# Kernel optimization log

Measured on AMD Instinct MI355X. Metric: run time of the kernel, lower is better.

## Reference

```python
import math
import jax, jax.numpy as jnp
import numpy as np

EMBED_DIM = 2048
NUM_HEADS = 16
DEPTH = 12
LAMBDA_INIT = 0.8 - 0.6 * math.exp(-0.3 * DEPTH)
LN_EPS = 1e-5


def setup_inputs() -> dict:
    key = jax.random.key(0)
    ks = jax.random.split(key, 9)
    D = EMBED_DIM
    hd = D // NUM_HEADS // 2  # 64
    B, T = 1, 2048
    w_std = D ** -0.5
    return {
        "x": jax.random.normal(ks[0], (B, T, D), jnp.float32),
        "Wq": jax.random.normal(ks[1], (D, D), jnp.float32) * w_std,
        "Wk": jax.random.normal(ks[2], (D, D), jnp.float32) * w_std,
        "Wv": jax.random.normal(ks[3], (D, D), jnp.float32) * w_std,
        "Wo": jax.random.normal(ks[4], (D, D), jnp.float32) * w_std,
        "lambda_q1": jax.random.normal(ks[5], (hd,), jnp.float32) * 0.1,
        "lambda_k1": jax.random.normal(ks[6], (hd,), jnp.float32) * 0.1,
        "lambda_q2": jax.random.normal(ks[7], (hd,), jnp.float32) * 0.1,
        "lambda_k2": jax.random.normal(ks[8], (hd,), jnp.float32) * 0.1,
    }


def reference(x, Wq, Wk, Wv, Wo, lambda_q1, lambda_k1, lambda_q2, lambda_k2):
    B, T, D = x.shape
    hd = lambda_q1.shape[0]
    H = D // (2 * hd)  # num_heads
    scale = hd ** -0.5

    # projections (torch Linear, no bias); n_rep == 1 so k/v are full width
    q = (x @ Wq).reshape(B, T, 2 * H, hd).transpose(0, 2, 1, 3) * scale  # (B,2H,T,hd)
    k = (x @ Wk).reshape(B, T, 2 * H, hd).transpose(0, 2, 1, 3)          # (B,2H,T,hd)
    v = (x @ Wv).reshape(B, T, H, 2 * hd).transpose(0, 2, 1, 3)          # (B,H,T,2hd)

    # dual-stream attention logits with causal mask (offset = 0)
    attn = jnp.einsum("bhqd,bhkd->bhqk", q, k)  # (B,2H,T,T)
    mask = jnp.triu(jnp.full((T, T), -jnp.inf, dtype=attn.dtype), 1)
    attn = jax.nn.softmax((attn + mask).astype(jnp.float32), axis=-1).astype(x.dtype)

    # lambda reparameterization
    lam1 = jnp.exp(jnp.sum(lambda_q1 * lambda_k1))
    lam2 = jnp.exp(jnp.sum(lambda_q2 * lambda_k2))
    lam = lam1 - lam2 + LAMBDA_INIT

    attn = attn.reshape(B, H, 2, T, T)
    diff = attn[:, :, 0] - lam * attn[:, :, 1]  # (B,H,T,T)
    out = jnp.einsum("bhqk,bhkd->bhqd", diff, v)  # (B,H,T,2hd)

    # subln: LayerNorm over last dim (2hd), no affine, biased variance
    mu = jnp.mean(out, axis=-1, keepdims=True)
    var = jnp.mean(jnp.square(out - mu), axis=-1, keepdims=True)
    out = (out - mu) / jnp.sqrt(var + LN_EPS)
    out = out * (1.0 - LAMBDA_INIT)

    # NOTE: faithful to original -- reshape WITHOUT transposing heads back
    out = out.reshape(B, T, H * 2 * hd)
    return out @ Wo
```

## Files before the change

kernel.cpp:

```cpp
#include <hip/hip_runtime.h>
#include <hip/hip_bf16.h>


typedef unsigned short u16;
typedef __attribute__((ext_vector_type(4))) float f32x4;
typedef __attribute__((ext_vector_type(8))) short bf16x8;

#define LAMBDA_INIT  0.7836057665317954f
#define ONE_MINUS_LI 0.2163942334682046f
#define QSCALE 0.18033688011112042f

#define EXP2F(x) __builtin_amdgcn_exp2f(x)

__device__ __forceinline__ u16 f2bf(float f) {
    union { float f; unsigned u; } v; v.f = f;
    unsigned r = v.u + 0x7FFFu + ((v.u >> 16) & 1u);
    return (u16)(r >> 16);
}

__device__ __forceinline__ unsigned pkbf(float a, float b) {
    union { __hip_bfloat162 h; unsigned u; } c;
    c.h = __float22bfloat162_rn(make_float2(a, b));
    return c.u;
}

__device__ __forceinline__ void gld_lds16(const u16* g, u16* l) {
    __builtin_amdgcn_global_load_lds((const __attribute__((address_space(1))) void*)g,
                                     (__attribute__((address_space(3))) void*)l, 16, 0, 0);
}

__global__ void cast_f32_bf16(const float* __restrict__ in, u16* __restrict__ out) {
    int i = (blockIdx.x * 256 + threadIdx.x) * 4;
    float4 v = *(const float4*)(in + i);
    uint2 o;
    o.x = pkbf(v.x, v.y);
    o.y = pkbf(v.z, v.w);
    *(uint2*)(out + i) = o;
}

__global__ void transpose_cast4(const float* __restrict__ W0, const float* __restrict__ W1,
                                const float* __restrict__ W2, const float* __restrict__ W3,
                                u16* __restrict__ O0, u16* __restrict__ O1,
                                u16* __restrict__ O2, u16* __restrict__ O3) {
    __shared__ float tile[64][65];
    const int z = blockIdx.z;
    const float* W = z == 0 ? W0 : z == 1 ? W1 : z == 2 ? W2 : W3;
    u16* Wt = z == 0 ? O0 : z == 1 ? O1 : z == 2 ? O2 : O3;
    const int c0 = blockIdx.x * 64, r0 = blockIdx.y * 64;
    const int t = threadIdx.x;
    const int lr = t >> 2, lc = (t & 3) << 4;
#pragma unroll
    for (int jj = 0; jj < 4; jj++) {
        float4 v = *(const float4*)(W + (size_t)(r0 + lr) * 2048 + c0 + lc + 4 * jj);
        tile[lr][lc + 4 * jj + 0] = v.x;
        tile[lr][lc + 4 * jj + 1] = v.y;
        tile[lr][lc + 4 * jj + 2] = v.z;
        tile[lr][lc + 4 * jj + 3] = v.w;
    }
    __syncthreads();
    const int oc = t >> 2, op = (t & 3) << 4;
    uint ou[8];
#pragma unroll
    for (int k = 0; k < 8; k++)
        ou[k] = pkbf(tile[op + 2 * k][oc], tile[op + 2 * k + 1][oc]);
    u16* dst = Wt + (size_t)(c0 + oc) * 2048 + r0 + op;
    *(uint4*)(dst) = *(uint4*)&ou[0];
    *(uint4*)(dst + 8) = *(uint4*)&ou[4];
}

__device__ __forceinline__ void gemm_core32(const u16* __restrict__ A, const u16* __restrict__ B,
                                            u16* __restrict__ Cout, float scale, int m0, int n0) {
    __shared__ __align__(16) u16 As[2][128 * 32];
    __shared__ __align__(16) u16 Bs[2][64 * 32];
    const int tid = threadIdx.x;
    const int lane = tid & 63, w = tid >> 6;
    const int q16 = lane & 15, g = lane >> 4;
    const int sl = (g ^ q16) & 3;
    const f32x4 fzero = {0.f, 0.f, 0.f, 0.f};
    f32x4 acc[2][4];
#pragma unroll
    for (int m = 0; m < 2; m++)
#pragma unroll
        for (int n = 0; n < 4; n++) acc[m][n] = fzero;

#define STG32(buf, kb)                                                               \
    {                                                                                \
        _Pragma("unroll") for (int p = 0; p < 2; p++) {                              \
            int s = p * 256 + tid;                              \
            int row = s >> 2, sg = (s ^ row) & 3;                                    \
            gld_lds16(A + (size_t)(m0 + row) * 2048 + (kb) + sg * 8, As[buf] + s * 8); \
        }                                                                            \
        {                                                                            \
            int s = tid;                                        \
            int row = s >> 2, sg = (s ^ row) & 3;                                    \
            gld_lds16(B + (size_t)(n0 + row) * 2048 + (kb) + sg * 8, Bs[buf] + s * 8); \
        }                                                                            \
    }

    STG32(0, 0);
    int cur = 0;
    for (int kb = 0; kb < 2048; kb += 32) {
        if (kb + 32 < 2048) {
            STG32(cur ^ 1, kb + 32);
            asm volatile("s_waitcnt vmcnt(3)" ::: "memory");
        } else {
            asm volatile("s_waitcnt vmcnt(0)" ::: "memory");
        }
        __builtin_amdgcn_s_barrier();
        bf16x8 af[2], bfr[4];
#pragma unroll
        for (int m = 0; m < 2; m++)
            af[m] = *(const bf16x8*)(As[cur] + (w * 32 + m * 16 + q16) * 32 + 8 * sl);
#pragma unroll
        for (int n = 0; n < 4; n++)
            bfr[n] = *(const bf16x8*)(Bs[cur] + (n * 16 + q16) * 32 + 8 * sl);
        __builtin_amdgcn_s_setprio(1);
#pragma unroll
        for (int m = 0; m < 2; m++)
#pragma unroll
            for (int n = 0; n < 4; n++)
                acc[m][n] = __builtin_amdgcn_mfma_f32_16x16x32_bf16(af[m], bfr[n], acc[m][n], 0, 0, 0);
        __builtin_amdgcn_s_setprio(0);
        asm volatile("s_waitcnt lgkmcnt(0)" ::: "memory");
        __builtin_amdgcn_s_barrier();
        cur ^= 1;
    }
#pragma unroll
    for (int m = 0; m < 2; m++)
#pragma unroll
        for (int n = 0; n < 4; n++) {
            int row = m0 + w * 32 + m * 16 + 4 * g;
            int col = n0 + n * 16 + q16;
#pragma unroll
            for (int r = 0; r < 4; r++)
                Cout[(size_t)(row + r) * 2048 + col] = f2bf(acc[m][n][r] * scale);
        }
#undef STG32
}

__device__ __forceinline__ void gemm_core64(const u16* __restrict__ A, const u16* __restrict__ B,
                                            float* __restrict__ Cout, float scale, int m0, int n0) {
    __shared__ __align__(16) u16 As[2][128 * 64];
    __shared__ __align__(16) u16 Bs[2][64 * 64];
    const int tid = threadIdx.x;
    const int lane = tid & 63, w = tid >> 6;
    const int q16 = lane & 15, g = lane >> 4;
    const int sw = q16 & 7;
    const f32x4 fzero = {0.f, 0.f, 0.f, 0.f};
    f32x4 acc[2][4];
#pragma unroll
    for (int m = 0; m < 2; m++)
#pragma unroll
        for (int n = 0; n < 4; n++) acc[m][n] = fzero;

#define STG64(buf, kb)                                                               \
    {                                                                                \
        _Pragma("unroll") for (int p = 0; p < 4; p++) {                              \
            int s = p * 256 + tid;                             \
            int row = s >> 3, sg = (s ^ row) & 7;                                    \
            gld_lds16(A + (size_t)(m0 + row) * 2048 + (kb) + sg * 8, As[buf] + s * 8); \
        }                                                                            \
        _Pragma("unroll") for (int p = 0; p < 2; p++) {                              \
            int s = p * 256 + tid;                              \
            int row = s >> 3, sg = (s ^ row) & 7;                                    \
            gld_lds16(B + (size_t)(n0 + row) * 2048 + (kb) + sg * 8, Bs[buf] + s * 8); \
        }                                                                            \
    }

    STG64(0, 0);
    int cur = 0;
    for (int kb = 0; kb < 2048; kb += 64) {
        if (kb + 64 < 2048) {
            STG64(cur ^ 1, kb + 64);
            asm volatile("s_waitcnt vmcnt(6)" ::: "memory");
        } else {
            asm volatile("s_waitcnt vmcnt(0)" ::: "memory");
        }
        __builtin_amdgcn_s_barrier();
        bf16x8 af[2][2], bfr[4][2];
#pragma unroll
        for (int m = 0; m < 2; m++) {
            const u16* ar = As[cur] + (w * 32 + m * 16 + q16) * 64;
            af[m][0] = *(const bf16x8*)(ar + 8 * (g ^ sw));
            af[m][1] = *(const bf16x8*)(ar + 8 * ((4 + g) ^ sw));
        }
#pragma unroll
        for (int n = 0; n < 4; n++) {
            const u16* br = Bs[cur] + (n * 16 + q16) * 64;
            bfr[n][0] = *(const bf16x8*)(br + 8 * (g ^ sw));
            bfr[n][1] = *(const bf16x8*)(br + 8 * ((4 + g) ^ sw));
        }
        __builtin_amdgcn_s_setprio(1);
#pragma unroll
        for (int m = 0; m < 2; m++)
#pragma unroll
            for (int n = 0; n < 4; n++) {
                acc[m][n] = __builtin_amdgcn_mfma_f32_16x16x32_bf16(af[m][0], bfr[n][0], acc[m][n], 0, 0, 0);
                acc[m][n] = __builtin_amdgcn_mfma_f32_16x16x32_bf16(af[m][1], bfr[n][1], acc[m][n], 0, 0, 0);
            }
        __builtin_amdgcn_s_setprio(0);
        asm volatile("s_waitcnt lgkmcnt(0)" ::: "memory");
        __builtin_amdgcn_s_barrier();
        cur ^= 1;
    }
#pragma unroll
    for (int m = 0; m < 2; m++)
#pragma unroll
        for (int n = 0; n < 4; n++) {
            int row = m0 + w * 32 + m * 16 + 4 * g;
            int col = n0 + n * 16 + q16;
#pragma unroll
            for (int r = 0; r < 4; r++)
                Cout[(size_t)(row + r) * 2048 + col] = acc[m][n][r] * scale;
        }
#undef STG64
}

__global__ __launch_bounds__(256, 6) void gemm_qkv(const u16* __restrict__ xb,
                                                   const u16* __restrict__ Wqt, const u16* __restrict__ Wkt,
                                                   const u16* __restrict__ Wvt,
                                                   u16* __restrict__ Qb, u16* __restrict__ Kb,
                                                   u16* __restrict__ Vtb) {
    const int id = blockIdx.x;
    const int ord = (id & 7) * 192 + (id >> 3);
    const int which = ord / 512, r = ord & 511;
    const int m0 = (r & 15) * 128, n0 = (r >> 4) * 64;
    const u16 *A, *B; u16* C; float sc;
    if (which == 0)      { A = xb;  B = Wqt; C = Qb;  sc = QSCALE; }
    else if (which == 1) { A = xb;  B = Wkt; C = Kb;  sc = 1.f; }
    else                 { A = Wvt; B = xb;  C = Vtb; sc = 1.f; }
    gemm_core32(A, B, C, sc, m0, n0);
}

__global__ __launch_bounds__(256, 3) void gemm_out(const u16* __restrict__ Mb, const u16* __restrict__ Wot,
                                                   float* __restrict__ out) {
    const int id = blockIdx.x;
    const int ord = (id & 7) * 64 + (id >> 3);
    const int m0 = (ord & 15) * 128, n0 = (ord >> 4) * 64;
    gemm_core64(Mb, Wot, out, 1.f, m0, n0);
}

__global__ __launch_bounds__(256, 2) void diff_attn(const u16* __restrict__ Qg, const u16* __restrict__ Kg,
                                                    const u16* __restrict__ Vg, u16* __restrict__ Mg,
                                                    const float* __restrict__ lq1, const float* __restrict__ lk1,
                                                    const float* __restrict__ lq2, const float* __restrict__ lk2) {
    __shared__ __align__(16) u16 smem[40960];
    const int tid = threadIdx.x;
    const int lane = tid & 63, w = tid >> 6;
    const int q16 = lane & 15, g = lane >> 4;
    const int sw = q16 & 7;
    const int id = blockIdx.x;
    const int xcd = id & 7, jj = id >> 3;
    const int p = jj >> 1, o = jj & 1;
    const int A = (p < 16) ? (32 - p) : (p - 15);
    const int s = o ? (33 - A) : A;
    const int qi = s - 1;
    const int h = (xcd << 1) | o;
    const int q0 = qi * 64;
    const int qg = q0 + 16 * w + q16;

    u16* Kb0 = smem;
    u16* Vb0 = smem + 8192;
    u16* Kb1 = smem + 16384;
    u16* Vb1 = smem + 24576;
    u16* Pw = smem + 32768 + w * 2048;

    bf16x8 qf[2][2];
#pragma unroll
    for (int st = 0; st < 2; st++)
#pragma unroll
        for (int db = 0; db < 2; db++)
            qf[st][db] = *(const bf16x8*)(Qg + (size_t)qg * 2048 + 128 * h + 64 * st + 32 * db + 8 * g);

#define STAGE_K(dst, kb)                                                         \
    {                                                                            \
        _Pragma("unroll") for (int p2 = 0; p2 < 4; p2++) {                       \
            int s2 = p2 * 256 + tid;                                             \
            int row = s2 >> 4, gc = s2 & 15;                                     \
            int sg = (gc ^ row) & 15;                                            \
            gld_lds16(Kg + (size_t)((kb) + row) * 2048 + 128 * h + sg * 8, (dst) + s2 * 8); \
        }                                                                        \
    }
#define STAGE_V(dst, kb)                                                         \
    {                                                                            \
        _Pragma("unroll") for (int p2 = 0; p2 < 4; p2++) {                       \
            int s2 = p2 * 256 + tid;                                             \
            int row = s2 >> 3, sg = (s2 ^ row) & 7;                              \
            gld_lds16(Vg + (size_t)(128 * h + row) * 2048 + (kb) + sg * 8, (dst) + s2 * 8); \
        }                                                                        \
    }

    const f32x4 fzero = {0.f, 0.f, 0.f, 0.f};
    f32x4 Oacc[2][8];
#pragma unroll
    for (int st = 0; st < 2; st++)
#pragma unroll
        for (int dt = 0; dt < 8; dt++) Oacc[st][dt] = fzero;
    float den[2] = {0.f, 0.f};

    const int nt = qi + 1;
    STAGE_K(Kb0, 0);
    STAGE_V(Vb0, 0);
    int cur = 0;
    for (int t = 0; t < nt; t++) {
        const int kb = t * 64;
        const u16* Ks = cur ? Kb1 : Kb0;
        const u16* Vs = cur ? Vb1 : Vb0;
        if (t + 1 < nt) {
            STAGE_K(cur ? Kb0 : Kb1, kb + 64);
            STAGE_V(cur ? Vb0 : Vb1, kb + 64);
            asm volatile("s_waitcnt vmcnt(8)" ::: "memory");
        } else {
            asm volatile("s_waitcnt vmcnt(0)" ::: "memory");
        }
        __builtin_amdgcn_s_barrier();

        f32x4 sc[2][4];
        __builtin_amdgcn_s_setprio(1);
#pragma unroll
        for (int st = 0; st < 2; st++)
#pragma unroll
            for (int kt = 0; kt < 4; kt++) {
                const u16* kr = Ks + (kt * 16 + q16) * 128;
                bf16x8 kf0 = *(const bf16x8*)(kr + 8 * ((st * 8 + g) ^ q16));
                bf16x8 kf1 = *(const bf16x8*)(kr + 8 * ((st * 8 + 4 + g) ^ q16));
                f32x4 a = __builtin_amdgcn_mfma_f32_16x16x32_bf16(kf0, qf[st][0], fzero, 0, 0, 0);
                a = __builtin_amdgcn_mfma_f32_16x16x32_bf16(kf1, qf[st][1], a, 0, 0, 0);
                sc[st][kt] = a;
            }
        __builtin_amdgcn_s_setprio(0);

        const bool last = (t == nt - 1);
#pragma unroll
        for (int st = 0; st < 2; st++) {
            u16* Pst = Pw + st * 1024;
            float dl = 0.f;
#pragma unroll
            for (int kt = 0; kt < 4; kt++) {
                float p0 = EXP2F(sc[st][kt][0]);
                float p1 = EXP2F(sc[st][kt][1]);
                float p2 = EXP2F(sc[st][kt][2]);
                float p3 = EXP2F(sc[st][kt][3]);
                if (last) {
                    const int kgi = kb + kt * 16 + 4 * g;
                    p0 = (kgi + 0 <= qg) ? p0 : 0.f;
                    p1 = (kgi + 1 <= qg) ? p1 : 0.f;
                    p2 = (kgi + 2 <= qg) ? p2 : 0.f;
                    p3 = (kgi + 3 <= qg) ? p3 : 0.f;
                }
                dl += (p0 + p1) + (p2 + p3);
                uint2 pr;
                pr.x = pkbf(p0, p1);
                pr.y = pkbf(p2, p3);
                *(uint2*)(Pst + q16 * 64 + ((kt * 16 + 4 * g) ^ (8 * sw))) = pr;
            }
            den[st] += dl;
        }

        bf16x8 pf[2][2];
#pragma unroll
        for (int st = 0; st < 2; st++)
#pragma unroll
            for (int kh = 0; kh < 2; kh++)
                pf[st][kh] = *(const bf16x8*)(Pw + st * 1024 + q16 * 64 + ((kh * 32 + 8 * g) ^ (8 * sw)));
        __builtin_amdgcn_s_setprio(1);
#pragma unroll
        for (int kh = 0; kh < 2; kh++)
#pragma unroll
            for (int dt = 0; dt < 8; dt++) {
                bf16x8 vf = *(const bf16x8*)(Vs + (dt * 16 + q16) * 64 + 8 * ((kh * 4 + g) ^ sw));
                Oacc[0][dt] = __builtin_amdgcn_mfma_f32_16x16x32_bf16(vf, pf[0][kh], Oacc[0][dt], 0, 0, 0);
                Oacc[1][dt] = __builtin_amdgcn_mfma_f32_16x16x32_bf16(vf, pf[1][kh], Oacc[1][dt], 0, 0, 0);
            }
        __builtin_amdgcn_s_setprio(0);
        asm volatile("s_waitcnt lgkmcnt(0)" ::: "memory");
        __builtin_amdgcn_s_barrier();
        cur ^= 1;
    }
#undef STAGE_K
#undef STAGE_V

    float sl1 = 0.f, sl2 = 0.f;
    for (int i = 0; i < 64; i++) { sl1 += lq1[i] * lk1[i]; sl2 += lq2[i] * lk2[i]; }
    const float lam = expf(sl1) - expf(sl2) + LAMBDA_INIT;

    float d0 = den[0], d1 = den[1];
    d0 += __shfl_xor(d0, 16); d0 += __shfl_xor(d0, 32);
    d1 += __shfl_xor(d1, 16); d1 += __shfl_xor(d1, 32);
    const float i1 = 1.f / d0;
    const float i2 = lam / d1;
    float S1 = 0.f, S2 = 0.f;
#pragma unroll
    for (int dt = 0; dt < 8; dt++)
#pragma unroll
        for (int r = 0; r < 4; r++) {
            float v = Oacc[0][dt][r] * i1 - Oacc[1][dt][r] * i2;
            S1 += v; S2 += v * v;
        }
    S1 += __shfl_xor(S1, 16); S1 += __shfl_xor(S1, 32);
    S2 += __shfl_xor(S2, 16); S2 += __shfl_xor(S2, 32);
    const float mu = S1 * (1.f / 128.f);
    const float var = S2 * (1.f / 128.f) - mu * mu;
    const float rs = rsqrtf(var + 1e-5f) * ONE_MINUS_LI;

    const int R = h * 128 + (q0 >> 4) + w;
    u16* drow = Mg + (size_t)R * 2048 + q16 * 128;
#pragma unroll
    for (int dt = 0; dt < 8; dt++) {
        float v0 = (Oacc[0][dt][0] * i1 - Oacc[1][dt][0] * i2 - mu) * rs;
        float v1 = (Oacc[0][dt][1] * i1 - Oacc[1][dt][1] * i2 - mu) * rs;
        float v2 = (Oacc[0][dt][2] * i1 - Oacc[1][dt][2] * i2 - mu) * rs;
        float v3 = (Oacc[0][dt][3] * i1 - Oacc[1][dt][3] * i2 - mu) * rs;
        uint2 oo;
        oo.x = pkbf(v0, v1);
        oo.y = pkbf(v2, v3);
        *(uint2*)(drow + dt * 16 + 4 * g) = oo;
    }
}

extern "C" void kernel_launch(void* const* d_in, const int* in_sizes, int n_in,
                              void* d_out, int out_size, void* d_ws, size_t ws_size,
                              hipStream_t stream) {
    (void)in_sizes; (void)n_in; (void)out_size; (void)ws_size;
    const float* x = (const float*)d_in[0];
    const float* Wq = (const float*)d_in[1];
    const float* Wk = (const float*)d_in[2];
    const float* Wv = (const float*)d_in[3];
    const float* Wo = (const float*)d_in[4];
    const float* lq1 = (const float*)d_in[5];
    const float* lk1 = (const float*)d_in[6];
    const float* lq2 = (const float*)d_in[7];
    const float* lk2 = (const float*)d_in[8];

    u16* ws = (u16*)d_ws;
    const size_t SZ = 2048u * 2048u;
    u16* xb = ws;
    u16* Wqt = ws + SZ;
    u16* Wkt = ws + 2 * SZ;
    u16* Wvt = ws + 3 * SZ;
    u16* Wot = ws + 4 * SZ;
    u16* Qb = ws + 5 * SZ;
    u16* Kb = ws + 6 * SZ;
    u16* Vtb = ws + 7 * SZ;
    u16* Mb = ws + 8 * SZ;

    cast_f32_bf16<<<4096, 256, 0, stream>>>(x, xb);
    transpose_cast4<<<dim3(32, 32, 4), 256, 0, stream>>>(Wq, Wk, Wv, Wo, Wqt, Wkt, Wvt, Wot);

    gemm_qkv<<<1536, 256, 0, stream>>>(xb, Wqt, Wkt, Wvt, Qb, Kb, Vtb);

    diff_attn<<<512, 256, 0, stream>>>(Qb, Kb, Vtb, Mb, lq1, lk1, lq2, lk2);

    gemm_out<<<512, 256, 0, stream>>>(Mb, Wot, (float*)d_out);
}
```

Baseline: 186.0 us.

## Enlarge QKV GEMM tile to 128x128 and fuse input cast into transpose kernel

The QKV projection GEMM moves from 128x64 to 128x128 output tiles, arranged as a 2x2 wave grid where each wave computes 64x64. This halves the block count and raises MFMA work per LDS load, which should improve operand reuse. It also changes the LDS swizzle and lowers the occupancy target. Separately, the x cast is folded into the weight transpose-cast kernel as an extra z-slice, saving one kernel launch. The cost is more registers per thread and lower occupancy.

```diff
diff --git a/kernel.cpp b/kernel.cpp
--- a/kernel.cpp
+++ b/kernel.cpp
@@ -29,26 +29,34 @@
                                      (__attribute__((address_space(3))) void*)l, 16, 0, 0);
 }
 
-__global__ void cast_f32_bf16(const float* __restrict__ in, u16* __restrict__ out) {
-    int i = (blockIdx.x * 256 + threadIdx.x) * 4;
-    float4 v = *(const float4*)(in + i);
-    uint2 o;
-    o.x = pkbf(v.x, v.y);
-    o.y = pkbf(v.z, v.w);
-    *(uint2*)(out + i) = o;
-}
-
-__global__ void transpose_cast4(const float* __restrict__ W0, const float* __restrict__ W1,
-                                const float* __restrict__ W2, const float* __restrict__ W3,
-                                u16* __restrict__ O0, u16* __restrict__ O1,
-                                u16* __restrict__ O2, u16* __restrict__ O3) {
+__global__ void prep_inputs(const float* __restrict__ x, const float* __restrict__ W0,
+                            const float* __restrict__ W1, const float* __restrict__ W2,
+                            const float* __restrict__ W3,
+                            u16* __restrict__ xb, u16* __restrict__ O0, u16* __restrict__ O1,
+                            u16* __restrict__ O2, u16* __restrict__ O3) {
     __shared__ float tile[64][65];
     const int z = blockIdx.z;
-    const float* W = z == 0 ? W0 : z == 1 ? W1 : z == 2 ? W2 : W3;
-    u16* Wt = z == 0 ? O0 : z == 1 ? O1 : z == 2 ? O2 : O3;
     const int c0 = blockIdx.x * 64, r0 = blockIdx.y * 64;
     const int t = threadIdx.x;
     const int lr = t >> 2, lc = (t & 3) << 4;
+
+    if (z == 4) {
+        const float* src = x + (size_t)(r0 + lr) * 2048 + c0 + lc;
+        uint ou[8];
+#pragma unroll
+        for (int jj = 0; jj < 4; jj++) {
+            float4 v = *(const float4*)(src + 4 * jj);
+            ou[2 * jj + 0] = pkbf(v.x, v.y);
+            ou[2 * jj + 1] = pkbf(v.z, v.w);
+        }
+        u16* dst = xb + (size_t)(r0 + lr) * 2048 + c0 + lc;
+        *(uint4*)(dst) = *(uint4*)&ou[0];
+        *(uint4*)(dst + 8) = *(uint4*)&ou[4];
+        return;
+    }
+
+    const float* W = z == 0 ? W0 : z == 1 ? W1 : z == 2 ? W2 : W3;
+    u16* Wt = z == 0 ? O0 : z == 1 ? O1 : z == 2 ? O2 : O3;
 #pragma unroll
     for (int jj = 0; jj < 4; jj++) {
         float4 v = *(const float4*)(W + (size_t)(r0 + lr) * 2048 + c0 + lc + 4 * jj);
@@ -68,55 +76,56 @@
     *(uint4*)(dst + 8) = *(uint4*)&ou[4];
 }
 
-__device__ __forceinline__ void gemm_core32(const u16* __restrict__ A, const u16* __restrict__ B,
+__device__ __forceinline__ void gemm_core_q(const u16* __restrict__ A, const u16* __restrict__ B,
                                             u16* __restrict__ Cout, float scale, int m0, int n0) {
     __shared__ __align__(16) u16 As[2][128 * 32];
-    __shared__ __align__(16) u16 Bs[2][64 * 32];
+    __shared__ __align__(16) u16 Bs[2][128 * 32];
     const int tid = threadIdx.x;
     const int lane = tid & 63, w = tid >> 6;
+    const int wr = w >> 1, wc = w & 1;
     const int q16 = lane & 15, g = lane >> 4;
-    const int sl = (g ^ q16) & 3;
     const f32x4 fzero = {0.f, 0.f, 0.f, 0.f};
-    f32x4 acc[2][4];
-#pragma unroll
-    for (int m = 0; m < 2; m++)
+    f32x4 acc[4][4];
+#pragma unroll
+    for (int m = 0; m < 4; m++)
 #pragma unroll
         for (int n = 0; n < 4; n++) acc[m][n] = fzero;
 
-#define STG32(buf, kb)                                                               \
+#define STGQ(buf, kb)                                                                \
     {                                                                                \
         _Pragma("unroll") for (int p = 0; p < 2; p++) {                              \
-            int s = p * 256 + tid;                              \
-            int row = s >> 2, sg = (s ^ row) & 3;                                    \
+            int s = p * 256 + tid;                \
+            int row = s >> 2, gc = s & 3;                                            \
+            int sg = (gc ^ (row >> 2)) & 3;                                          \
             gld_lds16(A + (size_t)(m0 + row) * 2048 + (kb) + sg * 8, As[buf] + s * 8); \
-        }                                                                            \
-        {                                                                            \
-            int s = tid;                                        \
-            int row = s >> 2, sg = (s ^ row) & 3;                                    \
             gld_lds16(B + (size_t)(n0 + row) * 2048 + (kb) + sg * 8, Bs[buf] + s * 8); \
         }                                                                            \
     }
 
-    STG32(0, 0);
+    STGQ(0, 0);
     int cur = 0;
     for (int kb = 0; kb < 2048; kb += 32) {
         if (kb + 32 < 2048) {
-            STG32(cur ^ 1, kb + 32);
-            asm volatile("s_waitcnt vmcnt(3)" ::: "memory");
+            STGQ(cur ^ 1, kb + 32);
+            asm volatile("s_waitcnt vmcnt(4)" ::: "memory");
         } else {
             asm volatile("s_waitcnt vmcnt(0)" ::: "memory");
         }
         __builtin_amdgcn_s_barrier();
-        bf16x8 af[2], bfr[4];
-#pragma unroll
-        for (int m = 0; m < 2; m++)
-            af[m] = *(const bf16x8*)(As[cur] + (w * 32 + m * 16 + q16) * 32 + 8 * sl);
-#pragma unroll
-        for (int n = 0; n < 4; n++)
-            bfr[n] = *(const bf16x8*)(Bs[cur] + (n * 16 + q16) * 32 + 8 * sl);
+        bf16x8 af[4], bfr[4];
+#pragma unroll
+        for (int m = 0; m < 4; m++) {
+            const int R = wr * 64 + m * 16 + q16;
+            af[m] = *(const bf16x8*)(As[cur] + R * 32 + 8 * ((g ^ (R >> 2)) & 3));
+        }
+#pragma unroll
+        for (int n = 0; n < 4; n++) {
+            const int R = wc * 64 + n * 16 + q16;
+            bfr[n] = *(const bf16x8*)(Bs[cur] + R * 32 + 8 * ((g ^ (R >> 2)) & 3));
+        }
         __builtin_amdgcn_s_setprio(1);
 #pragma unroll
-        for (int m = 0; m < 2; m++)
+        for (int m = 0; m < 4; m++)
 #pragma unroll
             for (int n = 0; n < 4; n++)
                 acc[m][n] = __builtin_amdgcn_mfma_f32_16x16x32_bf16(af[m], bfr[n], acc[m][n], 0, 0, 0);
@@ -126,16 +135,16 @@
         cur ^= 1;
     }
 #pragma unroll
-    for (int m = 0; m < 2; m++)
+    for (int m = 0; m < 4; m++)
 #pragma unroll
         for (int n = 0; n < 4; n++) {
-            int row = m0 + w * 32 + m * 16 + 4 * g;
-            int col = n0 + n * 16 + q16;
+            int row = m0 + wr * 64 + m * 16 + 4 * g;
+            int col = n0 + wc * 64 + n * 16 + q16;
 #pragma unroll
             for (int r = 0; r < 4; r++)
                 Cout[(size_t)(row + r) * 2048 + col] = f2bf(acc[m][n][r] * scale);
         }
-#undef STG32
+#undef STGQ
 }
 
 __device__ __forceinline__ void gemm_core64(const u16* __restrict__ A, const u16* __restrict__ B,
@@ -216,20 +225,20 @@
 #undef STG64
 }
 
-__global__ __launch_bounds__(256, 6) void gemm_qkv(const u16* __restrict__ xb,
+__global__ __launch_bounds__(256, 4) void gemm_qkv(const u16* __restrict__ xb,
                                                    const u16* __restrict__ Wqt, const u16* __restrict__ Wkt,
                                                    const u16* __restrict__ Wvt,
                                                    u16* __restrict__ Qb, u16* __restrict__ Kb,
                                                    u16* __restrict__ Vtb) {
     const int id = blockIdx.x;
-    const int ord = (id & 7) * 192 + (id >> 3);
-    const int which = ord / 512, r = ord & 511;
-    const int m0 = (r & 15) * 128, n0 = (r >> 4) * 64;
+    const int ord = (id & 7) * 96 + (id >> 3);
+    const int which = ord >> 8, r = ord & 255;
+    const int m0 = (r & 15) * 128, n0 = (r >> 4) * 128;
     const u16 *A, *B; u16* C; float sc;
     if (which == 0)      { A = xb;  B = Wqt; C = Qb;  sc = QSCALE; }
     else if (which == 1) { A = xb;  B = Wkt; C = Kb;  sc = 1.f; }
     else                 { A = Wvt; B = xb;  C = Vtb; sc = 1.f; }
-    gemm_core32(A, B, C, sc, m0, n0);
+    gemm_core_q(A, B, C, sc, m0, n0);
 }
 
 __global__ __launch_bounds__(256, 3) void gemm_out(const u16* __restrict__ Mb, const u16* __restrict__ Wot,
@@ -444,10 +453,9 @@
     u16* Vtb = ws + 7 * SZ;
     u16* Mb = ws + 8 * SZ;
 
-    cast_f32_bf16<<<4096, 256, 0, stream>>>(x, xb);
-    transpose_cast4<<<dim3(32, 32, 4), 256, 0, stream>>>(Wq, Wk, Wv, Wo, Wqt, Wkt, Wvt, Wot);
-
-    gemm_qkv<<<1536, 256, 0, stream>>>(xb, Wqt, Wkt, Wvt, Qb, Kb, Vtb);
+    prep_inputs<<<dim3(32, 32, 5), 256, 0, stream>>>(x, Wq, Wk, Wv, Wo, xb, Wqt, Wkt, Wvt, Wot);
+
+    gemm_qkv<<<768, 256, 0, stream>>>(xb, Wqt, Wkt, Wvt, Qb, Kb, Vtb);
 
     diff_attn<<<512, 256, 0, stream>>>(Qb, Kb, Vtb, Mb, lq1, lk1, lq2, lk2);
 
```

After: 164.3 us. 11.7% less time.
